# Optimization experiments

Measured on AMD Instinct MI355X. Metric: run time of the kernel, lower is better.

The kernel has to match this reference:

```python
import jax, jax.numpy as jnp
import numpy as np

B, IN, H = 8192, 2048, 2048


def setup_inputs() -> dict:
    key = jax.random.key(0)
    ks = jax.random.split(key, 8)
    inp = {
        "x_t": jax.random.normal(ks[0], (B, IN), dtype=jnp.float32),
        "h_prev": jax.random.normal(ks[1], (B, H), dtype=jnp.float32),
        "W_z": jax.random.normal(ks[2], (IN, H), dtype=jnp.float32) * 0.1,
        "W_r": jax.random.normal(ks[3], (IN, H), dtype=jnp.float32) * 0.1,
        "W_h": jax.random.normal(ks[4], (IN, H), dtype=jnp.float32) * 0.1,
        "U_z": jax.random.normal(ks[5], (H, H), dtype=jnp.float32) * 0.1,
        "U_r": jax.random.normal(ks[6], (H, H), dtype=jnp.float32) * 0.1,
        "U_h": jax.random.normal(ks[7], (H, H), dtype=jnp.float32) * 0.1,
        "b_z": jnp.zeros((H,), dtype=jnp.float32),
        "b_r": jnp.zeros((H,), dtype=jnp.float32),
        "b_h": jnp.zeros((H,), dtype=jnp.float32),
    }
    return inp


def reference(x_t, h_prev, W_z, W_r, W_h, U_z, U_r, U_h, b_z, b_r, b_h):
    # Batch the three input-side GEMMs and the two non-gated hidden-side GEMMs.
    Wx = x_t @ jnp.concatenate([W_z, W_r, W_h], axis=1)          # [B, 3H]
    Uh = h_prev @ jnp.concatenate([U_z, U_r], axis=1)            # [B, 2H]
    H_ = h_prev.shape[1]
    z_t = jax.nn.sigmoid(Wx[:, :H_] + Uh[:, :H_] + b_z)
    r_t = jax.nn.sigmoid(Wx[:, H_:2 * H_] + Uh[:, H_:] + b_r)
    # torch line `r_t * h_prev @ U_h` == (r_t * h_prev) @ U_h (left-to-right)
    h_tilda = jnp.tanh(Wx[:, 2 * H_:] + (r_t * h_prev) @ U_h + b_h)
    h_t = (1.0 - z_t) * h_prev + z_t * h_tilda
    return h_t
```

## Files before the change

kernel.cpp:

```cpp
#include <hip/hip_runtime.h>
#include <cstdint>
#include <cstddef>

#define B_DIM  8192
#define H_DIM  2048
#define LDA    6144
#define LDB    4096
#define NKT    64

typedef __attribute__((ext_vector_type(8))) short  short8;
typedef __attribute__((ext_vector_type(4))) float  float4v;

__device__ __forceinline__ unsigned short f2bf(float f) {
    union { float f; unsigned u; } v; v.f = f;
    unsigned r = v.u + 0x7fffu + ((v.u >> 16) & 1u);
    return (unsigned short)(r >> 16);
}

__device__ __forceinline__ float sigmoidf_(float x) {
    return 1.0f / (1.0f + __expf(-x));
}

#define AS1CV(p) ((const __attribute__((address_space(1))) void*)(p))
#define AS3V(p)  ((__attribute__((address_space(3))) void*)(p))

__global__ void cvt_rows(const float* __restrict__ x, const float* __restrict__ h,
                         unsigned short* __restrict__ Abuf) {
    const float* s = blockIdx.z ? h : x;
    const int coff = blockIdx.z ? 0 : 2048;
    const int row = blockIdx.x;
    const int c = threadIdx.x * 8;
    float4 a = *(const float4*)(s + (size_t)row * 2048 + c);
    float4 b = *(const float4*)(s + (size_t)row * 2048 + c + 4);
    union { unsigned short us[8]; uint4 u4; } o;
    o.us[0] = f2bf(a.x); o.us[1] = f2bf(a.y); o.us[2] = f2bf(a.z); o.us[3] = f2bf(a.w);
    o.us[4] = f2bf(b.x); o.us[5] = f2bf(b.y); o.us[6] = f2bf(b.z); o.us[7] = f2bf(b.w);
    *(uint4*)(Abuf + (size_t)row * LDA + coff + c) = o.u4;
}

struct P6 { const float* s[6]; unsigned short* d[6]; };

__global__ void transpose_cvt(P6 io) {
    __shared__ float tile[64][65];
    const float* src = io.s[blockIdx.z];
    unsigned short* dst = io.d[blockIdx.z];
    const int n0 = blockIdx.x * 64;
    const int k0 = blockIdx.y * 64;
    const int t = threadIdx.x;
#pragma unroll
    for (int p = 0; p < 4; ++p) {
        const int k = p * 16 + (t >> 4);
        const int n4 = (t & 15) * 4;
        float4 v = *(const float4*)(src + (size_t)(k0 + k) * 2048 + n0 + n4);
        tile[n4 + 0][k] = v.x; tile[n4 + 1][k] = v.y;
        tile[n4 + 2][k] = v.z; tile[n4 + 3][k] = v.w;
    }
    __syncthreads();
#pragma unroll
    for (int p = 0; p < 2; ++p) {
        const int n = p * 32 + (t >> 3);
        const int k8 = (t & 7) * 8;
        union { unsigned short us[8]; uint4 u4; } o;
#pragma unroll
        for (int q = 0; q < 8; ++q) o.us[q] = f2bf(tile[n][k8 + q]);
        *(uint4*)(dst + (size_t)(n0 + n) * LDB + k0 + k8) = o.u4;
    }
}

struct StagePtrs {
    const unsigned short* a0;
    const unsigned short* a1;
    const unsigned short* b0;
    const unsigned short* b1;
};

__device__ __constant__ const int kSlotDst[8] =
    {81920, 114688,    0, 32768, 16384, 49152, 65536, 98304};

template<int K, int OFF>
__device__ __forceinline__ void stage_slot(const StagePtrs& sp, char* lds, int t) {
    const unsigned short* s0 = (K & 1) ? sp.b0 : sp.a0;
    const unsigned short* s1 = (K & 1) ? sp.b1 : sp.a1;
    char* dst = lds + kSlotDst[K] + t * 16;
    __builtin_amdgcn_global_load_lds(AS1CV(s0 + OFF), AS3V(dst),        16, 0, 0);
    __builtin_amdgcn_global_load_lds(AS1CV(s1 + OFF), AS3V(dst + 8192), 16, 0, 0);
}

__device__ __forceinline__ void stage_item_pro(const StagePtrs& sp, char* lds, int t,
                                               int item) {
    const int tile = item >> 2;
    const int isB = item & 1;
    const int kh  = (item >> 1) & 1;
    const int sb  = tile & 1;
    const unsigned short* s0 = (isB ? sp.b0 : sp.a0) + tile * 64 + kh * 32;
    const unsigned short* s1 = (isB ? sp.b1 : sp.a1) + tile * 64 + kh * 32;
    char* dst = lds + sb * 65536 + isB * 32768 + kh * 16384 + t * 16;
    __builtin_amdgcn_global_load_lds(AS1CV(s0), AS3V(dst),        16, 0, 0);
    __builtin_amdgcn_global_load_lds(AS1CV(s1), AS3V(dst + 8192), 16, 0, 0);
}

struct Core8Ctx {
    char* lds;
    int t, aoff, wmb, wnb;
};

template<int K, int OFF, int MH, int NBUF, int NKK, int NMH, bool DOGATE>
__device__ __forceinline__ void phase5(const Core8Ctx& c, const StagePtrs& sp,
                                       short8 (&afc)[4], short8 (&afn)[4],
                                       short8 (&bfc)[4], short8 (&bfn)[4],
                                       float4v (&acc)[8][4]) {
    stage_slot<K, OFF>(sp, c.lds, c.t);
    {
        const char* abn = c.lds + (NBUF * 65536 + NKK * 16384) + c.wmb + c.aoff;
#pragma unroll
        for (int i = 0; i < 4; ++i)
            afn[i] = *(const short8*)(abn + (NMH * 4 + i) * 1024);
        if constexpr (NMH == 0) {
            const char* bbn = c.lds + (NBUF * 65536 + 32768 + NKK * 16384) + c.wnb + c.aoff;
#pragma unroll
            for (int j = 0; j < 4; ++j)
                bfn[j] = *(const short8*)(bbn + j * 1024);
        }
    }
    __builtin_amdgcn_sched_barrier(0);
    asm volatile("s_waitcnt lgkmcnt(%0)" :: "n"(NMH == 0 ? 8 : 4));
    __builtin_amdgcn_sched_barrier(0);
    __builtin_amdgcn_s_setprio(1);
#pragma unroll
    for (int i = 0; i < 4; ++i)
#pragma unroll
        for (int j = 0; j < 4; ++j)
            acc[MH * 4 + i][j] = __builtin_amdgcn_mfma_f32_16x16x32_bf16(
                afc[i], bfc[j], acc[MH * 4 + i][j], 0, 0, 0);
    __builtin_amdgcn_s_setprio(0);
    __builtin_amdgcn_sched_barrier(0);
    if constexpr (DOGATE) {
        asm volatile("s_waitcnt vmcnt(6)");
        __builtin_amdgcn_sched_barrier(0);
    }
    __builtin_amdgcn_s_barrier();
}

template<int O2, int O3, int O4, int O5, int O6, int O7>
__device__ __forceinline__ void iter8(const Core8Ctx& c, const StagePtrs& sp,
                                      short8 (&afA)[4], short8 (&afB)[4],
                                      short8 (&bfA)[4], short8 (&bfB)[4],
                                      float4v (&acc)[8][4]) {
    phase5<0,  96, 0, 0, 0, 1, false>(c, sp, afA, afB, bfA, bfB, acc);
    phase5<1,  96, 1, 0, 1, 0, true >(c, sp, afB, afA, bfA, bfB, acc);
    phase5<2, O2,  0, 0, 1, 1, false>(c, sp, afA, afB, bfB, bfA, acc);
    phase5<3, O3,  1, 1, 0, 0, true >(c, sp, afB, afA, bfB, bfA, acc);
    phase5<4, O4,  0, 1, 0, 1, false>(c, sp, afA, afB, bfA, bfB, acc);
    phase5<5, O5,  1, 1, 1, 0, true >(c, sp, afB, afA, bfA, bfB, acc);
    phase5<6, O6,  0, 1, 1, 1, false>(c, sp, afA, afB, bfB, bfA, acc);
    phase5<7, O7,  1, 0, 0, 0, true >(c, sp, afB, afA, bfB, bfA, acc);
}

__device__ __forceinline__ void gemm_core8(const unsigned short* __restrict__ Ag,
                                           const unsigned short* __restrict__ Bg,
                                           int m0, int n0, char* lds,
                                           float4v (&acc)[8][4]) {
    const int t    = threadIdx.x;
    const int lane = t & 63;
    const int wid  = t >> 6;
    Core8Ctx c;
    c.lds = lds; c.t = t;
    c.wmb = (wid >> 2) * 8192;
    c.wnb = (wid & 3) * 4096;
    const int fr  = lane & 15;
    const int seg = lane >> 4;
    c.aoff = (fr >> 1) * 128 + (((((fr & 1) << 2) | seg)) ^ ((fr >> 1) & 7)) * 16;
    const int sS   = (t & 7) ^ ((t >> 3) & 7);
    const int rowS = 2 * (t >> 3) + (sS >> 2);
    const int colS = (sS & 3) * 8;

    StagePtrs sp;
    sp.a0 = Ag + (size_t)(m0 + rowS) * LDA + colS;
    sp.a1 = sp.a0 + (size_t)128 * LDA;
    sp.b0 = Bg + (size_t)(n0 + rowS) * LDB + colS;
    sp.b1 = sp.b0 + (size_t)128 * LDB;

#pragma unroll
    for (int n = 0; n < 6; ++n) stage_item_pro(sp, lds, t, n);
    __builtin_amdgcn_sched_barrier(0);
    asm volatile("s_waitcnt vmcnt(4)");
    __builtin_amdgcn_sched_barrier(0);
    __builtin_amdgcn_s_barrier();

    short8 afA[4], afB[4], bfA[4], bfB[4];
    {
        const char* ab = c.lds + c.wmb + c.aoff;
#pragma unroll
        for (int i = 0; i < 4; ++i) afA[i] = *(const short8*)(ab + i * 1024);
        const char* bb = c.lds + 32768 + c.wnb + c.aoff;
#pragma unroll
        for (int j = 0; j < 4; ++j) bfA[j] = *(const short8*)(bb + j * 1024);
    }

    for (int it = 0; it < NKT / 2 - 1; ++it) {
        iter8<128, 128, 160, 160, 192, 192>(c, sp, afA, afB, bfA, bfB, acc);
        sp.a0 += 128; sp.a1 += 128; sp.b0 += 128; sp.b1 += 128;
    }
    iter8<0, 0, 0, 0, 0, 0>(c, sp, afA, afB, bfA, bfB, acc);
}

__global__ __launch_bounds__(512, 2) void gemm_zr(const unsigned short* __restrict__ Abuf,
                                                  const unsigned short* __restrict__ Bzr,
                                                  const float* __restrict__ hprev,
                                                  const float* __restrict__ bz,
                                                  const float* __restrict__ br,
                                                  float* __restrict__ zout,
                                                  unsigned short* __restrict__ Arh) {
    extern __shared__ char lds[];
    float4v acc[8][4];
#pragma unroll
    for (int i = 0; i < 8; ++i)
#pragma unroll
        for (int j = 0; j < 4; ++j)
            acc[i][j] = (float4v){0.f, 0.f, 0.f, 0.f};

    const int bid = blockIdx.x;
    const int x  = bid & 7;
    const int s  = bid >> 3;
    const int st = s >> 5;
    const int w  = s & 31;
    const int bm = (x >> 1) * 8 + st * 4 + (w & 3);
    const int bn = (x & 1) * 8 + (w >> 2);
    const int m0 = bm * 256;
    const int n0 = bn * 256;

    gemm_core8(Abuf, Bzr, m0, n0, lds, acc);

    const int t = threadIdx.x, lane = t & 63;
    const int wm = (t >> 6) >> 2, wn = (t >> 6) & 3;
    const int col = lane & 15, rbase = (lane >> 4) * 4;
    const bool zhalf = n0 < 2048;
#pragma unroll
    for (int i = 0; i < 8; ++i)
#pragma unroll
        for (int j = 0; j < 4; ++j) {
            const int gn = n0 + wn * 64 + j * 16 + col;
            const int gm0 = m0 + wm * 128 + i * 16 + rbase;
            if (zhalf) {
                const float bias = bz[gn];
#pragma unroll
                for (int r = 0; r < 4; ++r) {
                    const size_t idx = (size_t)(gm0 + r) * H_DIM + gn;
                    zout[idx] = sigmoidf_(acc[i][j][r] + bias);
                }
            } else {
                const int gn2 = gn - 2048;
                const float bias = br[gn2];
#pragma unroll
                for (int r = 0; r < 4; ++r) {
                    const size_t idx = (size_t)(gm0 + r) * H_DIM + gn2;
                    const float rt = sigmoidf_(acc[i][j][r] + bias);
                    Arh[(size_t)(gm0 + r) * LDA + gn2] = f2bf(rt * hprev[idx]);
                }
            }
        }
}

__global__ __launch_bounds__(512, 2) void gemm_h(const unsigned short* __restrict__ Axrh,
                                                 const unsigned short* __restrict__ Bh,
                                                 const float* __restrict__ hprev,
                                                 const float* __restrict__ bh,
                                                 float* __restrict__ out) {
    extern __shared__ char lds[];
    float4v acc[8][4];
#pragma unroll
    for (int i = 0; i < 8; ++i)
#pragma unroll
        for (int j = 0; j < 4; ++j)
            acc[i][j] = (float4v){0.f, 0.f, 0.f, 0.f};

    const int bid = blockIdx.x;
    const int x = bid & 7, s = bid >> 3;
    const int bm = x * 4 + (s & 3);
    const int bn = s >> 2;
    const int m0 = bm * 256;
    const int n0 = bn * 256;

    gemm_core8(Axrh, Bh, m0, n0, lds, acc);

    const int t = threadIdx.x, lane = t & 63;
    const int wm = (t >> 6) >> 2, wn = (t >> 6) & 3;
    const int col = lane & 15, rbase = (lane >> 4) * 4;
#pragma unroll
    for (int i = 0; i < 8; ++i)
#pragma unroll
        for (int j = 0; j < 4; ++j) {
            const int gn = n0 + wn * 64 + j * 16 + col;
            const int gm0 = m0 + wm * 128 + i * 16 + rbase;
            const float bias = bh[gn];
#pragma unroll
            for (int r = 0; r < 4; ++r) {
                const size_t idx = (size_t)(gm0 + r) * H_DIM + gn;
                const float ht = tanhf(acc[i][j][r] + bias);
                const float z = out[idx];
                const float h = hprev[idx];
                out[idx] = (1.0f - z) * h + z * ht;
            }
        }
}

extern "C" void kernel_launch(void* const* d_in, const int* in_sizes, int n_in,
                              void* d_out, int out_size, void* d_ws, size_t ws_size,
                              hipStream_t stream) {
    const float* x  = (const float*)d_in[0];
    const float* h  = (const float*)d_in[1];
    const float* Wz = (const float*)d_in[2];
    const float* Wr = (const float*)d_in[3];
    const float* Wh = (const float*)d_in[4];
    const float* Uz = (const float*)d_in[5];
    const float* Ur = (const float*)d_in[6];
    const float* Uh = (const float*)d_in[7];
    const float* bz = (const float*)d_in[8];
    const float* br = (const float*)d_in[9];
    const float* bh = (const float*)d_in[10];
    float* out = (float*)d_out;

    char* ws = (char*)d_ws;
    unsigned short* Abuf = (unsigned short*)(ws);
    unsigned short* Bzr  = (unsigned short*)(ws + (size_t)96  * 1024 * 1024);
    unsigned short* Bh   = (unsigned short*)(ws + (size_t)128 * 1024 * 1024);

    (void)hipFuncSetAttribute((const void*)gemm_zr,
                              hipFuncAttributeMaxDynamicSharedMemorySize, 131072);
    (void)hipFuncSetAttribute((const void*)gemm_h,
                              hipFuncAttributeMaxDynamicSharedMemorySize, 131072);

    cvt_rows<<<dim3(B_DIM, 1, 2), 256, 0, stream>>>(x, h, Abuf);

    P6 io;
    io.s[0] = Uz; io.d[0] = Bzr;
    io.s[1] = Wz; io.d[1] = Bzr + 2048;
    io.s[2] = Ur; io.d[2] = Bzr + (size_t)2048 * LDB;
    io.s[3] = Wr; io.d[3] = Bzr + (size_t)2048 * LDB + 2048;
    io.s[4] = Wh; io.d[4] = Bh;
    io.s[5] = Uh; io.d[5] = Bh + 2048;
    transpose_cvt<<<dim3(32, 32, 6), 256, 0, stream>>>(io);

    gemm_zr<<<dim3(512), dim3(512), 131072, stream>>>(Abuf, Bzr, h, bz, br, out,
                                                      Abuf + 4096 );

    gemm_h<<<dim3(256), dim3(512), 131072, stream>>>(Abuf + 2048 ,
                                                     Bh, h, bh, out);
}
```

Measured before the change: 697.5 us.

## Remove LDS fragment double-buffering; load fragments in-phase before MFMA

Removes the register-level ping-pong of A/B fragments, where each phase prefetched the next phase's LDS fragments while computing the current one. Each phase now reads its own fragments from LDS, issues the global-to-LDS staging, waits at a barrier, drains lgkmcnt fully and then runs the MFMAs. This frees the registers held by the second fragment set, which could ease register pressure at 2 blocks per CU. The cost is that LDS read latency is no longer hidden behind MFMA work. The prologue wait is loosened to vmcnt(8) because the first fragments are no longer read ahead of the loop.

```diff
diff --git a/kernel.cpp b/kernel.cpp
--- a/kernel.cpp
+++ b/kernel.cpp
@@ -104,26 +104,27 @@
     int t, aoff, wmb, wnb;
 };
 
-template<int K, int OFF, int MH, int NBUF, int NKK, int NMH, bool DOGATE>
-__device__ __forceinline__ void phase5(const Core8Ctx& c, const StagePtrs& sp,
-                                       short8 (&afc)[4], short8 (&afn)[4],
-                                       short8 (&bfc)[4], short8 (&bfn)[4],
-                                       float4v (&acc)[8][4]) {
+template<int K, int OFF, bool DOGATE>
+__device__ __forceinline__ void phase6(const Core8Ctx& c, const StagePtrs& sp,
+                                       short8 (&bf_)[4], float4v (&acc)[8][4]) {
+    constexpr int BUF = K >> 2, KK = (K >> 1) & 1, MH = K & 1;
+    short8 af[4];
+    {
+        const char* ab = c.lds + (BUF * 65536 + KK * 16384) + c.wmb + c.aoff;
+#pragma unroll
+        for (int i = 0; i < 4; ++i)
+            af[i] = *(const short8*)(ab + (MH * 4 + i) * 1024);
+        if constexpr (MH == 0) {
+            const char* bb = c.lds + (BUF * 65536 + 32768 + KK * 16384) + c.wnb + c.aoff;
+#pragma unroll
+            for (int j = 0; j < 4; ++j)
+                bf_[j] = *(const short8*)(bb + j * 1024);
+        }
+    }
     stage_slot<K, OFF>(sp, c.lds, c.t);
-    {
-        const char* abn = c.lds + (NBUF * 65536 + NKK * 16384) + c.wmb + c.aoff;
-#pragma unroll
-        for (int i = 0; i < 4; ++i)
-            afn[i] = *(const short8*)(abn + (NMH * 4 + i) * 1024);
-        if constexpr (NMH == 0) {
-            const char* bbn = c.lds + (NBUF * 65536 + 32768 + NKK * 16384) + c.wnb + c.aoff;
-#pragma unroll
-            for (int j = 0; j < 4; ++j)
-                bfn[j] = *(const short8*)(bbn + j * 1024);
-        }
-    }
-    __builtin_amdgcn_sched_barrier(0);
-    asm volatile("s_waitcnt lgkmcnt(%0)" :: "n"(NMH == 0 ? 8 : 4));
+    __builtin_amdgcn_sched_barrier(0);
+    __builtin_amdgcn_s_barrier();
+    asm volatile("s_waitcnt lgkmcnt(0)");
     __builtin_amdgcn_sched_barrier(0);
     __builtin_amdgcn_s_setprio(1);
 #pragma unroll
@@ -131,7 +132,7 @@
 #pragma unroll
         for (int j = 0; j < 4; ++j)
             acc[MH * 4 + i][j] = __builtin_amdgcn_mfma_f32_16x16x32_bf16(
-                afc[i], bfc[j], acc[MH * 4 + i][j], 0, 0, 0);
+                af[i], bf_[j], acc[MH * 4 + i][j], 0, 0, 0);
     __builtin_amdgcn_s_setprio(0);
     __builtin_amdgcn_sched_barrier(0);
     if constexpr (DOGATE) {
@@ -143,17 +144,15 @@
 
 template<int O2, int O3, int O4, int O5, int O6, int O7>
 __device__ __forceinline__ void iter8(const Core8Ctx& c, const StagePtrs& sp,
-                                      short8 (&afA)[4], short8 (&afB)[4],
-                                      short8 (&bfA)[4], short8 (&bfB)[4],
-                                      float4v (&acc)[8][4]) {
-    phase5<0,  96, 0, 0, 0, 1, false>(c, sp, afA, afB, bfA, bfB, acc);
-    phase5<1,  96, 1, 0, 1, 0, true >(c, sp, afB, afA, bfA, bfB, acc);
-    phase5<2, O2,  0, 0, 1, 1, false>(c, sp, afA, afB, bfB, bfA, acc);
-    phase5<3, O3,  1, 1, 0, 0, true >(c, sp, afB, afA, bfB, bfA, acc);
-    phase5<4, O4,  0, 1, 0, 1, false>(c, sp, afA, afB, bfA, bfB, acc);
-    phase5<5, O5,  1, 1, 1, 0, true >(c, sp, afB, afA, bfA, bfB, acc);
-    phase5<6, O6,  0, 1, 1, 1, false>(c, sp, afA, afB, bfB, bfA, acc);
-    phase5<7, O7,  1, 0, 0, 0, true >(c, sp, afB, afA, bfB, bfA, acc);
+                                      short8 (&bf_)[4], float4v (&acc)[8][4]) {
+    phase6<0,  96, false>(c, sp, bf_, acc);
+    phase6<1,  96, true >(c, sp, bf_, acc);
+    phase6<2, O2,  false>(c, sp, bf_, acc);
+    phase6<3, O3,  true >(c, sp, bf_, acc);
+    phase6<4, O4,  false>(c, sp, bf_, acc);
+    phase6<5, O5,  true >(c, sp, bf_, acc);
+    phase6<6, O6,  false>(c, sp, bf_, acc);
+    phase6<7, O7,  true >(c, sp, bf_, acc);
 }
 
 __device__ __forceinline__ void gemm_core8(const unsigned short* __restrict__ Ag,
@@ -183,25 +182,16 @@
 #pragma unroll
     for (int n = 0; n < 6; ++n) stage_item_pro(sp, lds, t, n);
     __builtin_amdgcn_sched_barrier(0);
-    asm volatile("s_waitcnt vmcnt(4)");
+    asm volatile("s_waitcnt vmcnt(8)");
     __builtin_amdgcn_sched_barrier(0);
     __builtin_amdgcn_s_barrier();
 
-    short8 afA[4], afB[4], bfA[4], bfB[4];
-    {
-        const char* ab = c.lds + c.wmb + c.aoff;
-#pragma unroll
-        for (int i = 0; i < 4; ++i) afA[i] = *(const short8*)(ab + i * 1024);
-        const char* bb = c.lds + 32768 + c.wnb + c.aoff;
-#pragma unroll
-        for (int j = 0; j < 4; ++j) bfA[j] = *(const short8*)(bb + j * 1024);
-    }
-
+    short8 bf_[4];
     for (int it = 0; it < NKT / 2 - 1; ++it) {
-        iter8<128, 128, 160, 160, 192, 192>(c, sp, afA, afB, bfA, bfB, acc);
+        iter8<128, 128, 160, 160, 192, 192>(c, sp, bf_, acc);
         sp.a0 += 128; sp.a1 += 128; sp.b0 += 128; sp.b1 += 128;
     }
-    iter8<0, 0, 0, 0, 0, 0>(c, sp, afA, afB, bfA, bfB, acc);
+    iter8<0, 0, 0, 0, 0, 0>(c, sp, bf_, acc);
 }
 
 __global__ __launch_bounds__(512, 2) void gemm_zr(const unsigned short* __restrict__ Abuf,
```

Result: no change. 702.4 us (+0.7%).
